# Performance work log

Measured on AMD Instinct MI355X. Metric: run time of the kernel, lower is better.

The kernel has to match this reference:

```python
import jax, jax.numpy as jnp
import numpy as np

V, E, HID, L = 32000, 2048, 8192, 4
H, KV, DK, DH = 16, 4, 128, 128
SEQ, WINDOW = 2048, 1024
EPS = 1e-5


def rms_norm(x):
    return x * jax.lax.rsqrt(jnp.mean(x * x, axis=-1, keepdims=True) + EPS)


def rope_buffers(seq_len, key_size):
    half = key_size // 2
    offset = jnp.arange(key_size) % half
    scales = jnp.power(10000.0, -2.0 / key_size * offset.astype(jnp.float32))
    angles = jnp.arange(seq_len, dtype=jnp.float32)[:, None] * scales[None, :]  # [S, DK]
    cos = jnp.cos(angles)
    sin = jnp.sin(angles)
    sin = sin.at[:, :half].multiply(-1.0)
    return cos, sin


def rotate(f, cos, sin):
    # f: [B, heads, S, DK]; cos/sin: [S, DK]
    half = DK // 2
    swapped = jnp.concatenate([f[..., half:], f[..., :half]], axis=-1)
    return cos * f + sin * swapped


def sliding_window_attention(q, k, v, window):
    # q: [B,H,S,DK], k: [B,KV,S,DK], v: [B,KV,S,DH]; GQA broadcast
    B, _, S, _ = q.shape
    G = H // KV
    qg = q.reshape(B, KV, G, S, DK)
    scores = jnp.einsum('bkgqd,bkjd->bkgqj', qg, k) / jnp.sqrt(jnp.asarray(DK, q.dtype))
    i = jnp.arange(S)[:, None]
    j = jnp.arange(S)[None, :]
    mask = (j <= i) & (i - j < window)
    scores = jnp.where(mask, scores, jnp.asarray(-1e9, scores.dtype))
    probs = jax.nn.softmax(scores, axis=-1)
    out = jnp.einsum('bkgqj,bkjd->bkgqd', probs, v)
    return out.reshape(B, H, S, DH)


def setup_inputs() -> dict:
    key = jax.random.key(0)
    ks = jax.random.split(key, 9)
    s = lambda k, shape, fan: jax.random.normal(k, shape, jnp.float32) / np.sqrt(fan)
    return {
        'tokens': jax.random.randint(ks[0], (1, SEQ), 0, V),
        'table': jax.random.normal(ks[1], (V, E), jnp.float32) * 0.02,
        'wq': s(ks[2], (L, E, H * DK), E),
        'wk': s(ks[3], (L, E, KV * DK), E),
        'wv': s(ks[4], (L, E, KV * DH), E),
        'wo': s(ks[5], (L, H * DH, E), H * DH),
        'w_up': s(ks[6], (L, E, 2 * HID), E),
        'w_down': s(ks[7], (L, HID, E), HID),
        'w_vocab': s(ks[8], (E, V), E),
    }


def reference(tokens, table, wq, wk, wv, wo, w_up, w_down, w_vocab):
    B, S = tokens.shape
    table = table.at[0].set(0.0)  # forward zeroes row 0 each call
    cos, sin = rope_buffers(S, DK)
    x = table[tokens]  # [B, S, E]
    for l in range(L):
        # --- self attention ---
        n = rms_norm(x)
        q = (n @ wq[l]).reshape(B, S, H, DK).transpose(0, 2, 1, 3)
        k = (n @ wk[l]).reshape(B, S, KV, DK).transpose(0, 2, 1, 3)
        v = (n @ wv[l]).reshape(B, S, KV, DH).transpose(0, 2, 1, 3)
        q = rotate(q, cos, sin)
        k = rotate(k, cos, sin)
        attn = sliding_window_attention(q, k, v, WINDOW)
        attn = attn.transpose(0, 2, 1, 3).reshape(B, S, H * DH)
        x = x + attn @ wo[l]
        # --- SwiGLU FFN ---
        n = rms_norm(x)
        gu = n @ w_up[l]
        gate, up = gu[..., :HID], gu[..., HID:]
        x = x + (up * jax.nn.silu(gate)) @ w_down[l]
    x = rms_norm(x)
    logits = x @ w_vocab  # [B, S, V]
    return logits
```

## Files before the change

### kernel.cpp

```cpp
#include <hip/hip_runtime.h>
#include <cstdint>

typedef unsigned short bf16u;
typedef __attribute__((ext_vector_type(8))) short short8;
typedef __attribute__((ext_vector_type(4))) short short4v;
typedef __attribute__((ext_vector_type(4))) float f32x4;

#define SEQ   2048
#define EMB   2048
#define NHEAD 16
#define NKV   4
#define DKH   128
#define HIDN  8192
#define NVOC  32000
#define NLAY  4
#define WIN   1024
#define QKV_N 3072

__device__ __forceinline__ bf16u f2bf(float f) {
  union { float f; uint32_t u; } v; v.f = f;
  uint32_t r = v.u + 0x7FFFu + ((v.u >> 16) & 1u);
  return (bf16u)(r >> 16);
}
__device__ __forceinline__ float bf2f(bf16u b) {
  union { uint32_t u; float f; } v; v.u = ((uint32_t)b) << 16;
  return v.f;
}

__device__ __forceinline__ void gl2lds16(const void* g, void* l) {
  __builtin_amdgcn_global_load_lds(
      (const __attribute__((address_space(1))) void*)g,
      (__attribute__((address_space(3))) void*)l, 16, 0, 0);
}

__global__ __launch_bounds__(256) void embed_kernel(const int* __restrict__ tokens,
                                                    const float* __restrict__ table,
                                                    float* __restrict__ x) {
  int s = blockIdx.x;
  int tok = tokens[s];
  int i0 = threadIdx.x * 8;
  float4 a = {0,0,0,0}, b = {0,0,0,0};
  if (tok != 0) {
    const float* src = table + (size_t)tok * EMB;
    a = *(const float4*)(src + i0);
    b = *(const float4*)(src + i0 + 4);
  }
  *(float4*)(x + (size_t)s * EMB + i0) = a;
  *(float4*)(x + (size_t)s * EMB + i0 + 4) = b;
}

__global__ __launch_bounds__(256) void rmsnorm_kernel(const float* __restrict__ x,
                                                      bf16u* __restrict__ out) {
  int s = blockIdx.x;
  const float* row = x + (size_t)s * EMB;
  int i0 = threadIdx.x * 8;
  float4 a = *(const float4*)(row + i0);
  float4 b = *(const float4*)(row + i0 + 4);
  float ss = a.x*a.x + a.y*a.y + a.z*a.z + a.w*a.w
           + b.x*b.x + b.y*b.y + b.z*b.z + b.w*b.w;
  #pragma unroll
  for (int off = 1; off < 64; off <<= 1) ss += __shfl_xor(ss, off);
  __shared__ float red[4];
  if ((threadIdx.x & 63) == 0) red[threadIdx.x >> 6] = ss;
  __syncthreads();
  float scale = rsqrtf((red[0] + red[1] + red[2] + red[3]) * (1.0f / EMB) + 1e-5f);
  float v[8] = {a.x, a.y, a.z, a.w, b.x, b.y, b.z, b.w};
  short8 o;
  #pragma unroll
  for (int j = 0; j < 8; ++j) o[j] = (short)f2bf(v[j] * scale);
  *(short8*)(out + (size_t)s * EMB + i0) = o;
}

__global__ __launch_bounds__(256) void reduce4norm_kernel(float* __restrict__ x,
                                                          const float* __restrict__ p,
                                                          bf16u* __restrict__ nout) {
  int s = blockIdx.x;
  const size_t MN = (size_t)SEQ * EMB;
  size_t base = (size_t)s * EMB + threadIdx.x * 8;
  float v[8];
  #pragma unroll
  for (int h = 0; h < 2; ++h) {
    size_t i = base + h * 4;
    float4 a  = *(const float4*)(x + i);
    float4 b0 = *(const float4*)(p + i);
    float4 b1 = *(const float4*)(p + i + MN);
    float4 b2 = *(const float4*)(p + i + 2 * MN);
    float4 b3 = *(const float4*)(p + i + 3 * MN);
    v[h*4+0] = a.x + b0.x + b1.x + b2.x + b3.x;
    v[h*4+1] = a.y + b0.y + b1.y + b2.y + b3.y;
    v[h*4+2] = a.z + b0.z + b1.z + b2.z + b3.z;
    v[h*4+3] = a.w + b0.w + b1.w + b2.w + b3.w;
    *(float4*)(x + i) = make_float4(v[h*4+0], v[h*4+1], v[h*4+2], v[h*4+3]);
  }
  float ss = 0.0f;
  #pragma unroll
  for (int j = 0; j < 8; ++j) ss += v[j] * v[j];
  #pragma unroll
  for (int off = 1; off < 64; off <<= 1) ss += __shfl_xor(ss, off);
  __shared__ float red[4];
  if ((threadIdx.x & 63) == 0) red[threadIdx.x >> 6] = ss;
  __syncthreads();
  float scale = rsqrtf((red[0] + red[1] + red[2] + red[3]) * (1.0f / EMB) + 1e-5f);
  short8 o;
  #pragma unroll
  for (int j = 0; j < 8; ++j) o[j] = (short)f2bf(v[j] * scale);
  *(short8*)(nout + base) = o;
}

__global__ __launch_bounds__(256) void transp_kernel(const float* __restrict__ in,
                                                     bf16u* __restrict__ out,
                                                     int R, int C, int pairhalf,
                                                     size_t ostride) {
  __shared__ float tile[64][65];
  in  += (size_t)blockIdx.z * R * C;
  out += (size_t)blockIdx.z * ostride;
  int c0 = blockIdx.x * 64, r0 = blockIdx.y * 64;
  int tx = threadIdx.x & 15, ty = threadIdx.x >> 4;
  #pragma unroll
  for (int i = 0; i < 4; ++i) {
    int r = ty + i * 16;
    float4 v = *(const float4*)(in + (size_t)(r0 + r) * C + c0 + tx * 4);
    tile[tx * 4 + 0][r] = v.x;
    tile[tx * 4 + 1][r] = v.y;
    tile[tx * 4 + 2][r] = v.z;
    tile[tx * 4 + 3][r] = v.w;
  }
  __syncthreads();
  int rx = threadIdx.x & 15, cy = threadIdx.x >> 4;
  #pragma unroll
  for (int i = 0; i < 4; ++i) {
    int c = c0 + cy + i * 16;
    int n = pairhalf ? (c < pairhalf ? 2 * c : 2 * (c - pairhalf) + 1) : c;
    short4v o;
    #pragma unroll
    for (int j = 0; j < 4; ++j) o[j] = (short)f2bf(tile[cy + i * 16][rx * 4 + j]);
    *(short4v*)(out + (size_t)n * R + r0 + rx * 4) = o;
  }
}

__global__ __launch_bounds__(256) void rope_kernel(const bf16u* __restrict__ qkv,
                                                   bf16u* __restrict__ q_bf,
                                                   bf16u* __restrict__ k_bf) {
  int idx = blockIdx.x * 256 + threadIdx.x;
  int d = idx & 63;
  int s = (idx >> 6) & (SEQ - 1);
  int h = idx >> 17;
  int col0 = (h < NHEAD) ? h * DKH : 2048 + (h - NHEAD) * DKH;
  const bf16u* row = qkv + (size_t)s * QKV_N + col0;
  float ang = (float)s * __powf(10000.0f, -(float)d * (1.0f / 64.0f));
  float si, c;
  sincosf(ang, &si, &c);
  float f0 = bf2f(row[d]), f1 = bf2f(row[d + 64]);
  bf16u* orow = (h < NHEAD) ? q_bf + ((size_t)h * SEQ + s) * DKH
                            : k_bf + ((size_t)(h - NHEAD) * SEQ + s) * DKH;
  orow[d]      = f2bf(c * f0 - si * f1);
  orow[d + 64] = f2bf(c * f1 + si * f0);
}

template <int MODE>
__global__ __launch_bounds__(256) void gemm_kernel(const bf16u* __restrict__ A,
                                                   const bf16u* __restrict__ Bt,
                                                   void* __restrict__ C,
                                                   int M, int N, int K) {
  __shared__ __align__(16) char lds[2][2][8192];

  int nx = gridDim.x, ny = gridDim.y;
  int nwg = nx * ny;
  int orig = blockIdx.y * nx + blockIdx.x;
  int q = nwg >> 3, r = nwg & 7;
  int xcd = orig & 7, loc = orig >> 3;
  int id = (xcd < r ? xcd * (q + 1) : r * (q + 1) + (xcd - r) * q) + loc;
  int bx = id / ny, by = id - bx * ny;
  int n0 = bx * 128, m0 = by * 128;

  int t = threadIdx.x;
  int w = t >> 6, l = t & 63;
  int wm = (w >> 1) * 64, wn = (w & 1) * 64;
  int l15 = l & 15, l4 = l >> 4;

  int srow = w * 16 + (l >> 2);
  int scol = (l & 3) * 8;

  f32x4 acc[4][4] = {};

  auto stage = [&](int buf, int k0) {
    #pragma unroll
    for (int i = 0; i < 2; ++i) {
      gl2lds16(A  + (size_t)(m0 + i * 64 + srow) * K + k0 + scol,
               &lds[buf][0][i * 4096 + w * 1024]);
      gl2lds16(Bt + (size_t)(n0 + i * 64 + srow) * K + k0 + scol,
               &lds[buf][1][i * 4096 + w * 1024]);
    }
  };

  auto compute = [&](int buf) {
    short8 af[4], bfr[4];
    #pragma unroll
    for (int i = 0; i < 4; ++i) {
      af[i]  = *(const short8*)(&lds[buf][0][((wm + i * 16 + l15) * 32 + l4 * 8) * 2]);
      bfr[i] = *(const short8*)(&lds[buf][1][((wn + i * 16 + l15) * 32 + l4 * 8) * 2]);
    }
    #pragma unroll
    for (int i = 0; i < 4; ++i)
      #pragma unroll
      for (int j = 0; j < 4; ++j)
        acc[i][j] = __builtin_amdgcn_mfma_f32_16x16x32_bf16(af[i], bfr[j], acc[i][j], 0, 0, 0);
  };

  int nt = K >> 5;
  int cur = 0;
  stage(0, 0);
  __syncthreads();
  for (int tt = 0; tt < nt; ++tt) {
    if (tt + 1 < nt) stage(cur ^ 1, (tt + 1) * 32);
    compute(cur);
    __syncthreads();
    cur ^= 1;
  }

  #pragma unroll
  for (int i = 0; i < 4; ++i)
    #pragma unroll
    for (int j = 0; j < 4; ++j) {
      int col = n0 + wn + j * 16 + l15;
      #pragma unroll
      for (int rr = 0; rr < 4; ++rr) {
        int row = m0 + wm + i * 16 + l4 * 4 + rr;
        float v = acc[i][j][rr];
        if (MODE == 0) {
          ((bf16u*)C)[(size_t)row * N + col] = f2bf(v);
        } else if (MODE == 1) {
          float* p = (float*)C + (size_t)row * N + col;
          *p += v;
        } else {
          ((float*)C)[(size_t)row * N + col] = v;
        }
      }
    }
}

__device__ __forceinline__ void stage_half(const bf16u* __restrict__ p, int ld,
                                           int row0, int k0, char* slotBase, int t) {
  int r  = t >> 3, c8 = t & 7;
  int cs = (c8 ^ (r & 7)) << 3;
  gl2lds16(p + (size_t)(row0 + r) * ld + k0 + cs, slotBase + t * 16);
  gl2lds16(p + (size_t)(row0 + 64 + r) * ld + k0 + cs, slotBase + 8192 + t * 16);
}

template<int KK>
__device__ __forceinline__ short8 read_frag(const char* slot, int row, int l4) {
  int kc = KK * 4 + l4;
  return *(const short8*)(slot + row * 128 + ((kc ^ (row & 7)) << 4));
}

template<int NH>
__device__ __forceinline__ void mfma_quad(f32x4 (&acc)[8][4], const short8 (&a)[8],
                                          short8 b0, short8 b1) {
  __builtin_amdgcn_s_setprio(1);
  #pragma unroll
  for (int mi = 0; mi < 8; ++mi) {
    acc[mi][NH * 2]     = __builtin_amdgcn_mfma_f32_16x16x32_bf16(a[mi], b0, acc[mi][NH * 2], 0, 0, 0);
    acc[mi][NH * 2 + 1] = __builtin_amdgcn_mfma_f32_16x16x32_bf16(a[mi], b1, acc[mi][NH * 2 + 1], 0, 0, 0);
  }
  __builtin_amdgcn_s_setprio(0);
}

template <int MODE>
__global__ __launch_bounds__(512) void gemm256_kernel(const bf16u* __restrict__ A,
                                                      const bf16u* __restrict__ Bt,
                                                      void* __restrict__ C,
                                                      int M, int N, int K, int ldk) {
  __shared__ __align__(16) char lds[131072];

  int koff = blockIdx.z * K;
  A  += koff;
  Bt += koff;
  float* Cz = (float*)C + (size_t)blockIdx.z * M * N;

  int nx = gridDim.x, ny = gridDim.y;
  int nwg = nx * ny;
  int orig = blockIdx.y * nx + blockIdx.x;
  int q8 = nwg >> 3, r8 = nwg & 7;
  int xcd = orig & 7, loc = orig >> 3;
  int id = (xcd < r8 ? xcd * (q8 + 1) : r8 * (q8 + 1) + (xcd - r8) * q8) + loc;
  int bx = id / ny, by = id - bx * ny;
  int n0 = bx * 256, m0 = by * 256;

  int t = threadIdx.x;
  int wid = t >> 6, lane = t & 63;
  int wr = wid >> 2, wc = wid & 3, bh = wc >> 1;
  int l15 = lane & 15, l4 = lane >> 4;

  char* AS0 = lds;              char* AS1 = lds + 16384;
  char* AS2 = lds + 32768;      char* AS3 = lds + 49152;
  char* BS0 = lds + 65536;      char* BS1 = lds + 81920;
  char* BS2 = lds + 98304;      char* BS3 = lds + 114688;

  const char* ASe = lds + wr * 16384;
  const char* ASo = ASe + 32768;
  const char* BSe = lds + 65536 + bh * 16384;
  const char* BSo = BSe + 32768;

  int brow = (wc & 1) * 64;

  f32x4 acc[8][4] = {};
  short8 a[8];
  short8 b0, b1;

  int NT = K >> 6;
  int NI = NT >> 1;

  stage_half(A,  ldk, m0,       0,  AS0, t);
  stage_half(A,  ldk, m0 + 128, 0,  AS1, t);
  stage_half(Bt, ldk, n0,       0,  BS0, t);
  stage_half(Bt, ldk, n0 + 128, 0,  BS1, t);
  stage_half(A,  ldk, m0,       64, AS2, t);
  asm volatile("s_waitcnt vmcnt(2)" ::: "memory");
  __builtin_amdgcn_s_barrier();
  __builtin_amdgcn_sched_barrier(0);

  for (int I = 0; I < NI; ++I) {
    int t0k = I * 128;
    int t1k = t0k + 64;
    bool notlast = (I + 1 < NI);

    #pragma unroll
    for (int mi = 0; mi < 8; ++mi) a[mi] = read_frag<0>(ASe, mi * 16 + l15, l4);
    b0 = read_frag<0>(BSe, brow + l15, l4);
    b1 = read_frag<0>(BSe, brow + 16 + l15, l4);
    stage_half(A, ldk, m0 + 128, t1k, AS3, t);
    __builtin_amdgcn_s_barrier();
    mfma_quad<0>(acc, a, b0, b1);
    __builtin_amdgcn_s_barrier();

    b0 = read_frag<0>(BSe, brow + 32 + l15, l4);
    b1 = read_frag<0>(BSe, brow + 48 + l15, l4);
    stage_half(Bt, ldk, n0, t1k, BS2, t);
    __builtin_amdgcn_s_barrier();
    mfma_quad<1>(acc, a, b0, b1);
    __builtin_amdgcn_s_barrier();

    #pragma unroll
    for (int mi = 0; mi < 8; ++mi) a[mi] = read_frag<1>(ASe, mi * 16 + l15, l4);
    b0 = read_frag<1>(BSe, brow + l15, l4);
    b1 = read_frag<1>(BSe, brow + 16 + l15, l4);
    stage_half(Bt, ldk, n0 + 128, t1k, BS3, t);
    __builtin_amdgcn_s_barrier();
    mfma_quad<0>(acc, a, b0, b1);
    __builtin_amdgcn_s_barrier();

    b0 = read_frag<1>(BSe, brow + 32 + l15, l4);
    b1 = read_frag<1>(BSe, brow + 48 + l15, l4);
    if (notlast) stage_half(A, ldk, m0, t0k + 128, AS0, t);
    if (notlast) { asm volatile("s_waitcnt vmcnt(2)" ::: "memory"); }
    else         { asm volatile("s_waitcnt vmcnt(0)" ::: "memory"); }
    __builtin_amdgcn_s_barrier();
    __builtin_amdgcn_sched_barrier(0);
    mfma_quad<1>(acc, a, b0, b1);
    __builtin_amdgcn_s_barrier();

    #pragma unroll
    for (int mi = 0; mi < 8; ++mi) a[mi] = read_frag<0>(ASo, mi * 16 + l15, l4);
    b0 = read_frag<0>(BSo, brow + l15, l4);
    b1 = read_frag<0>(BSo, brow + 16 + l15, l4);
    if (notlast) stage_half(A, ldk, m0 + 128, t0k + 128, AS1, t);
    __builtin_amdgcn_s_barrier();
    mfma_quad<0>(acc, a, b0, b1);
    __builtin_amdgcn_s_barrier();

    b0 = read_frag<0>(BSo, brow + 32 + l15, l4);
    b1 = read_frag<0>(BSo, brow + 48 + l15, l4);
    if (notlast) stage_half(Bt, ldk, n0, t0k + 128, BS0, t);
    __builtin_amdgcn_s_barrier();
    mfma_quad<1>(acc, a, b0, b1);
    __builtin_amdgcn_s_barrier();

    #pragma unroll
    for (int mi = 0; mi < 8; ++mi) a[mi] = read_frag<1>(ASo, mi * 16 + l15, l4);
    b0 = read_frag<1>(BSo, brow + l15, l4);
    b1 = read_frag<1>(BSo, brow + 16 + l15, l4);
    if (notlast) stage_half(Bt, ldk, n0 + 128, t0k + 128, BS1, t);
    __builtin_amdgcn_s_barrier();
    mfma_quad<0>(acc, a, b0, b1);
    __builtin_amdgcn_s_barrier();

    b0 = read_frag<1>(BSo, brow + 32 + l15, l4);
    b1 = read_frag<1>(BSo, brow + 48 + l15, l4);
    if (notlast) {
      stage_half(A, ldk, m0, t0k + 192, AS2, t);
      asm volatile("s_waitcnt vmcnt(2)" ::: "memory");
    }
    __builtin_amdgcn_s_barrier();
    __builtin_amdgcn_sched_barrier(0);
    mfma_quad<1>(acc, a, b0, b1);
    __builtin_amdgcn_s_barrier();
  }

  #pragma unroll
  for (int mi = 0; mi < 8; ++mi)
    #pragma unroll
    for (int ni = 0; ni < 4; ++ni) {
      int col = n0 + wc * 64 + ni * 16 + l15;
      #pragma unroll
      for (int rr = 0; rr < 4; ++rr) {
        int row = m0 + wr * 128 + mi * 16 + l4 * 4 + rr;
        float v = acc[mi][ni][rr];
        if (MODE == 3) {
          float pv = __shfl_xor(v, 1);
          if ((l15 & 1) == 0) {
            float hval = pv * (v / (1.0f + __expf(-v)));
            ((bf16u*)C)[(size_t)row * HIDN + (col >> 1)] = f2bf(hval);
          }
        } else if (MODE == 2) {
          Cz[(size_t)row * N + col] = v;
        } else if (MODE == 1) {
          float* p = (float*)C + (size_t)row * N + col;
          *p += v;
        } else {
          ((bf16u*)C)[(size_t)row * N + col] = f2bf(v);
        }
      }
    }
}

__global__ __launch_bounds__(512) void attn_kernel(const bf16u* __restrict__ q_bf,
                                                   const bf16u* __restrict__ k_bf,
                                                   const bf16u* __restrict__ qkv_bf,
                                                   bf16u* __restrict__ attn_out) {
  int h = blockIdx.y;
  int q0 = blockIdx.x * 128;
  int kvh = h >> 2;
  const bf16u* Kp = k_bf + (size_t)kvh * SEQ * DKH;
  const bf16u* Vp = qkv_bf + 2560 + kvh * DKH;

  __shared__ __align__(16) char  Klds[64 * 128 * 2];
  __shared__ __align__(16) bf16u Vlds[128][72];
  __shared__ __align__(16) bf16u Plds[8][16][72];

  int t = threadIdx.x, wave = t >> 6, lane = t & 63;
  int l15 = lane & 15, l4 = lane >> 4;
  int qrow0 = q0 + wave * 16;

  short8 qf[4];
  #pragma unroll
  for (int ks = 0; ks < 4; ++ks)
    qf[ks] = *(const short8*)(q_bf + ((size_t)h * SEQ + qrow0 + l15) * DKH + ks * 32 + l4 * 8);

  f32x4 o[8] = {};
  float m[4], lsum[4];
  #pragma unroll
  for (int r = 0; r < 4; ++r) { m[r] = -INFINITY; lsum[r] = 0.0f; }

  int vkey = t & 63, vd0 = (t >> 6) * 16;

  int jstart = q0 >= WIN ? ((q0 - (WIN - 1)) & ~63) : 0;

  for (int j0 = jstart; j0 < q0 + 128; j0 += 64) {
    __syncthreads();
    #pragma unroll
    for (int i = 0; i < 2; ++i) {
      int c = t + i * 512;
      int key = c >> 4, cc = c & 15;
      int off = key * 256 + cc * 16; off ^= (key & 7) << 4;
      *(short8*)(Klds + off) = *(const short8*)(Kp + (size_t)(j0 + key) * DKH + cc * 8);
    }
    {
      const bf16u* src = Vp + (size_t)(j0 + vkey) * QKV_N + vd0;
      short8 v0 = *(const short8*)(src);
      short8 v1 = *(const short8*)(src + 8);
      #pragma unroll
      for (int i = 0; i < 8; ++i) Vlds[vd0 + i][vkey] = (bf16u)(unsigned short)v0[i];
      #pragma unroll
      for (int i = 0; i < 8; ++i) Vlds[vd0 + 8 + i][vkey] = (bf16u)(unsigned short)v1[i];
    }
    __syncthreads();

    f32x4 sacc[4] = {};
    #pragma unroll
    for (int nt = 0; nt < 4; ++nt) {
      int key = nt * 16 + l15;
      #pragma unroll
      for (int ks = 0; ks < 4; ++ks) {
        int off = key * 256 + ks * 64 + l4 * 16; off ^= (key & 7) << 4;
        short8 kf = *(short8*)(Klds + off);
        sacc[nt] = __builtin_amdgcn_mfma_f32_16x16x32_bf16(qf[ks], kf, sacc[nt], 0, 0, 0);
      }
    }

    float sv[4][4];
    #pragma unroll
    for (int nt = 0; nt < 4; ++nt) {
      int jk = j0 + nt * 16 + l15;
      #pragma unroll
      for (int r = 0; r < 4; ++r) {
        int iq = qrow0 + l4 * 4 + r;
        float s = sacc[nt][r] * 0.08838834764831845f;
        bool valid = (jk <= iq) && (iq - jk < WIN);
        sv[nt][r] = valid ? s : -1e9f;
      }
    }

    float mxr[4];
    #pragma unroll
    for (int r = 0; r < 4; ++r) {
      float mx = fmaxf(fmaxf(sv[0][r], sv[1][r]), fmaxf(sv[2][r], sv[3][r]));
      #pragma unroll
      for (int off = 1; off < 16; off <<= 1) mx = fmaxf(mx, __shfl_xor(mx, off));
      mxr[r] = mx;
    }

    bool grow = (mxr[0] > m[0] + 8.0f) || (mxr[1] > m[1] + 8.0f) ||
                (mxr[2] > m[2] + 8.0f) || (mxr[3] > m[3] + 8.0f);
    if (__any(grow)) {
      #pragma unroll
      for (int r = 0; r < 4; ++r) {
        float mn = fmaxf(m[r], mxr[r]);
        float alpha = __expf(m[r] - mn);
        m[r] = mn;
        lsum[r] *= alpha;
        #pragma unroll
        for (int d = 0; d < 8; ++d) o[d][r] *= alpha;
      }
    }

    float p[4][4];
    #pragma unroll
    for (int r = 0; r < 4; ++r) {
      float ps = 0.0f;
      #pragma unroll
      for (int nt = 0; nt < 4; ++nt) { p[nt][r] = __expf(sv[nt][r] - m[r]); ps += p[nt][r]; }
      #pragma unroll
      for (int off = 1; off < 16; off <<= 1) ps += __shfl_xor(ps, off);
      lsum[r] += ps;
    }

    #pragma unroll
    for (int nt = 0; nt < 4; ++nt)
      #pragma unroll
      for (int r = 0; r < 4; ++r)
        Plds[wave][l4 * 4 + r][nt * 16 + l15] = f2bf(p[nt][r]);

    #pragma unroll
    for (int kk = 0; kk < 2; ++kk) {
      short8 pf = *(short8*)(&Plds[wave][l15][kk * 32 + l4 * 8]);
      #pragma unroll
      for (int d = 0; d < 8; ++d) {
        short8 vf = *(short8*)(&Vlds[d * 16 + l15][kk * 32 + l4 * 8]);
        o[d] = __builtin_amdgcn_mfma_f32_16x16x32_bf16(pf, vf, o[d], 0, 0, 0);
      }
    }
  }

  #pragma unroll
  for (int d = 0; d < 8; ++d)
    #pragma unroll
    for (int r = 0; r < 4; ++r) {
      int row = qrow0 + l4 * 4 + r;
      attn_out[(size_t)row * (NHEAD * DKH) + h * DKH + d * 16 + l15] = f2bf(o[d][r] / lsum[r]);
    }
}

extern "C" void kernel_launch(void* const* d_in, const int* in_sizes, int n_in,
                              void* d_out, int out_size, void* d_ws, size_t ws_size,
                              hipStream_t stream) {
  const int*   tokens  = (const int*)d_in[0];
  const float* table   = (const float*)d_in[1];
  const float* wq      = (const float*)d_in[2];
  const float* wk      = (const float*)d_in[3];
  const float* wv      = (const float*)d_in[4];
  const float* wo      = (const float*)d_in[5];
  const float* w_up    = (const float*)d_in[6];
  const float* w_down  = (const float*)d_in[7];
  const float* w_vocab = (const float*)d_in[8];
  float* out = (float*)d_out;

  char* base = (char*)d_ws;
  size_t o = 0;
  auto alloc = [&](size_t bytes) { size_t r = o; o += (bytes + 255) & ~(size_t)255; return r; };
  size_t o_x     = alloc((size_t)SEQ * EMB * 4);
  size_t o_nbf   = alloc((size_t)SEQ * EMB * 2);
  size_t o_qkvw  = alloc((size_t)NLAY * QKV_N * EMB * 2);
  size_t o_wot   = alloc((size_t)NLAY * EMB * EMB * 2);
  size_t o_wupt  = alloc((size_t)NLAY * 2 * HIDN * EMB * 2);
  size_t o_wdnt  = alloc((size_t)NLAY * EMB * HIDN * 2);
  size_t o_qkvbf = alloc((size_t)SEQ * QKV_N * 2);
  size_t o_qbf   = alloc((size_t)NHEAD * SEQ * DKH * 2);
  size_t o_kbf   = alloc((size_t)NKV * SEQ * DKH * 2);
  size_t o_attn  = alloc((size_t)SEQ * EMB * 2);
  size_t o_big   = alloc((size_t)SEQ * 2 * HIDN * 4);
  size_t o_hbf   = alloc((size_t)SEQ * HIDN * 2);

  float* x      = (float*)(base + o_x);
  bf16u* n_bf   = (bf16u*)(base + o_nbf);
  bf16u* qkvw_t = (bf16u*)(base + o_qkvw);
  bf16u* wo_t   = (bf16u*)(base + o_wot);
  bf16u* wup_t  = (bf16u*)(base + o_wupt);
  bf16u* wdn_t  = (bf16u*)(base + o_wdnt);
  bf16u* qkv_bf = (bf16u*)(base + o_qkvbf);
  bf16u* q_bf   = (bf16u*)(base + o_qbf);
  bf16u* k_bf   = (bf16u*)(base + o_kbf);
  bf16u* attn_b = (bf16u*)(base + o_attn);
  float* part   = (float*)(base + o_big);
  bf16u* h_bf   = (bf16u*)(base + o_hbf);
  bf16u* wvoc_t = (bf16u*)(base + o_big);

  const size_t QKVW = (size_t)QKV_N * EMB;

  transp_kernel<<<dim3(EMB / 64, EMB / 64, NLAY), 256, 0, stream>>>(
      wq, qkvw_t, EMB, EMB, 0, QKVW);
  transp_kernel<<<dim3(512 / 64, EMB / 64, NLAY), 256, 0, stream>>>(
      wk, qkvw_t + (size_t)2048 * EMB, EMB, 512, 0, QKVW);
  transp_kernel<<<dim3(512 / 64, EMB / 64, NLAY), 256, 0, stream>>>(
      wv, qkvw_t + (size_t)2560 * EMB, EMB, 512, 0, QKVW);
  transp_kernel<<<dim3(EMB / 64, EMB / 64, NLAY), 256, 0, stream>>>(
      wo, wo_t, EMB, EMB, 0, (size_t)EMB * EMB);
  transp_kernel<<<dim3(2 * HIDN / 64, EMB / 64, NLAY), 256, 0, stream>>>(
      w_up, wup_t, EMB, 2 * HIDN, HIDN, (size_t)2 * HIDN * EMB);
  transp_kernel<<<dim3(EMB / 64, HIDN / 64, NLAY), 256, 0, stream>>>(
      w_down, wdn_t, HIDN, EMB, 0, (size_t)EMB * HIDN);

  embed_kernel<<<SEQ, 256, 0, stream>>>(tokens, table, x);
  rmsnorm_kernel<<<SEQ, 256, 0, stream>>>(x, n_bf);

  for (int l = 0; l < NLAY; ++l) {
    gemm_kernel<0><<<dim3(QKV_N / 128, SEQ / 128), 256, 0, stream>>>(
        n_bf, qkvw_t + (size_t)l * QKVW, qkv_bf, SEQ, QKV_N, EMB);

    rope_kernel<<<(NHEAD + NKV) * SEQ * 64 / 256, 256, 0, stream>>>(qkv_bf, q_bf, k_bf);

    attn_kernel<<<dim3(SEQ / 128, NHEAD), 512, 0, stream>>>(q_bf, k_bf, qkv_bf, attn_b);

    gemm_kernel<1><<<dim3(EMB / 128, SEQ / 128), 256, 0, stream>>>(
        attn_b, wo_t + (size_t)l * EMB * EMB, x, SEQ, EMB, EMB);

    rmsnorm_kernel<<<SEQ, 256, 0, stream>>>(x, n_bf);
    gemm256_kernel<3><<<dim3(2 * HIDN / 256, SEQ / 256), 512, 0, stream>>>(
        n_bf, wup_t + (size_t)l * 2 * HIDN * EMB, h_bf, SEQ, 2 * HIDN, EMB, EMB);
    gemm256_kernel<2><<<dim3(EMB / 256, SEQ / 256, 4), 512, 0, stream>>>(
        h_bf, wdn_t + (size_t)l * EMB * HIDN, part, SEQ, EMB, 2048, HIDN);
    reduce4norm_kernel<<<SEQ, 256, 0, stream>>>(x, part, n_bf);
  }

  transp_kernel<<<dim3(NVOC / 64, EMB / 64, 1), 256, 0, stream>>>(
      w_vocab, wvoc_t, EMB, NVOC, 0, 0);
  gemm256_kernel<2><<<dim3(NVOC / 256, SEQ / 256), 512, 0, stream>>>(
      n_bf, wvoc_t, out, SEQ, NVOC, EMB, EMB);
}
```

Before: 2.349 ms.

## Fuse RoPE into attention, precompute rope table, split KV range across two blocks

Removes the separate rope kernel. A sin/cos table is now computed once per forward, and the rotation is applied to Q and K as they are loaded inside the attention kernel. Attention now splits each query tile's key range into two halves along a new grid z dimension, which doubles the number of blocks. Each block writes unnormalized fp32 partial outputs plus max and sum statistics, and a new combine kernel merges them into bf16. The cost is extra fp32 partial traffic, one extra launch per layer, and K being re-rotated by every head that shares it.

Result: slower. 2.399 ms (+2.1%).

```diff
diff --git a/kernel.cpp b/kernel.cpp
--- a/kernel.cpp
+++ b/kernel.cpp
@@ -47,6 +47,17 @@
   }
   *(float4*)(x + (size_t)s * EMB + i0) = a;
   *(float4*)(x + (size_t)s * EMB + i0 + 4) = b;
+}
+
+__global__ __launch_bounds__(256) void ropetab_kernel(float* __restrict__ tab) {
+  int idx = blockIdx.x * 256 + threadIdx.x;
+  int d = idx & 63;
+  int s = idx >> 6;
+  float ang = (float)s * __powf(10000.0f, -(float)d * (1.0f / 64.0f));
+  float si, c;
+  sincosf(ang, &si, &c);
+  tab[(size_t)s * 128 + d] = c;
+  tab[(size_t)s * 128 + 64 + d] = si;
 }
 
 __global__ __launch_bounds__(256) void rmsnorm_kernel(const float* __restrict__ x,
@@ -136,25 +147,6 @@
     for (int j = 0; j < 4; ++j) o[j] = (short)f2bf(tile[cy + i * 16][rx * 4 + j]);
     *(short4v*)(out + (size_t)n * R + r0 + rx * 4) = o;
   }
-}
-
-__global__ __launch_bounds__(256) void rope_kernel(const bf16u* __restrict__ qkv,
-                                                   bf16u* __restrict__ q_bf,
-                                                   bf16u* __restrict__ k_bf) {
-  int idx = blockIdx.x * 256 + threadIdx.x;
-  int d = idx & 63;
-  int s = (idx >> 6) & (SEQ - 1);
-  int h = idx >> 17;
-  int col0 = (h < NHEAD) ? h * DKH : 2048 + (h - NHEAD) * DKH;
-  const bf16u* row = qkv + (size_t)s * QKV_N + col0;
-  float ang = (float)s * __powf(10000.0f, -(float)d * (1.0f / 64.0f));
-  float si, c;
-  sincosf(ang, &si, &c);
-  float f0 = bf2f(row[d]), f1 = bf2f(row[d + 64]);
-  bf16u* orow = (h < NHEAD) ? q_bf + ((size_t)h * SEQ + s) * DKH
-                            : k_bf + ((size_t)(h - NHEAD) * SEQ + s) * DKH;
-  orow[d]      = f2bf(c * f0 - si * f1);
-  orow[d + 64] = f2bf(c * f1 + si * f0);
 }
 
 template <int MODE>
@@ -423,15 +415,16 @@
     }
 }
 
-__global__ __launch_bounds__(512) void attn_kernel(const bf16u* __restrict__ q_bf,
-                                                   const bf16u* __restrict__ k_bf,
-                                                   const bf16u* __restrict__ qkv_bf,
-                                                   bf16u* __restrict__ attn_out) {
+__global__ __launch_bounds__(512) void attn_kernel(const bf16u* __restrict__ qkv_bf,
+                                                   const float* __restrict__ tab,
+                                                   float* __restrict__ opart,
+                                                   float* __restrict__ mlbuf) {
   int h = blockIdx.y;
   int q0 = blockIdx.x * 128;
+  int z = blockIdx.z;
   int kvh = h >> 2;
-  const bf16u* Kp = k_bf + (size_t)kvh * SEQ * DKH;
-  const bf16u* Vp = qkv_bf + 2560 + kvh * DKH;
+  const bf16u* Kg = qkv_bf + 2048 + kvh * DKH;
+  const bf16u* Vg = qkv_bf + 2560 + kvh * DKH;
 
   __shared__ __align__(16) char  Klds[64 * 128 * 2];
   __shared__ __align__(16) bf16u Vlds[128][72];
@@ -441,10 +434,32 @@
   int l15 = lane & 15, l4 = lane >> 4;
   int qrow0 = q0 + wave * 16;
 
+  int qrow = qrow0 + l15;
   short8 qf[4];
-  #pragma unroll
-  for (int ks = 0; ks < 4; ++ks)
-    qf[ks] = *(const short8*)(q_bf + ((size_t)h * SEQ + qrow0 + l15) * DKH + ks * 32 + l4 * 8);
+  {
+    short8 qr[4];
+    #pragma unroll
+    for (int ks = 0; ks < 4; ++ks)
+      qr[ks] = *(const short8*)(qkv_bf + (size_t)qrow * QKV_N + h * DKH + ks * 32 + l4 * 8);
+    #pragma unroll
+    for (int hf = 0; hf < 2; ++hf) {
+      int dbase = hf * 32 + l4 * 8;
+      const float* tc = tab + (size_t)qrow * 128 + dbase;
+      float4 c0 = *(const float4*)(tc);
+      float4 c1 = *(const float4*)(tc + 4);
+      float4 s0 = *(const float4*)(tc + 64);
+      float4 s1 = *(const float4*)(tc + 68);
+      float cc[8] = {c0.x,c0.y,c0.z,c0.w,c1.x,c1.y,c1.z,c1.w};
+      float ssn[8] = {s0.x,s0.y,s0.z,s0.w,s1.x,s1.y,s1.z,s1.w};
+      #pragma unroll
+      for (int j = 0; j < 8; ++j) {
+        float f0 = bf2f((bf16u)(unsigned short)qr[hf][j]);
+        float f1 = bf2f((bf16u)(unsigned short)qr[hf + 2][j]);
+        qf[hf][j]     = (short)f2bf(cc[j] * f0 - ssn[j] * f1);
+        qf[hf + 2][j] = (short)f2bf(cc[j] * f1 + ssn[j] * f0);
+      }
+    }
+  }
 
   f32x4 o[8] = {};
   float m[4], lsum[4];
@@ -452,20 +467,43 @@
   for (int r = 0; r < 4; ++r) { m[r] = -INFINITY; lsum[r] = 0.0f; }
 
   int vkey = t & 63, vd0 = (t >> 6) * 16;
+  int kkey = t & 63, kd0 = (t >> 6) * 8;
 
   int jstart = q0 >= WIN ? ((q0 - (WIN - 1)) & ~63) : 0;
-
-  for (int j0 = jstart; j0 < q0 + 128; j0 += 64) {
+  int T  = (q0 + 128 - jstart) >> 6;
+  int T0 = T >> 1;
+  int jb = jstart + (z ? T0 * 64 : 0);
+  int je = z ? (jstart + T * 64) : (jstart + T0 * 64);
+
+  for (int j0 = jb; j0 < je; j0 += 64) {
     __syncthreads();
-    #pragma unroll
-    for (int i = 0; i < 2; ++i) {
-      int c = t + i * 512;
-      int key = c >> 4, cc = c & 15;
-      int off = key * 256 + cc * 16; off ^= (key & 7) << 4;
-      *(short8*)(Klds + off) = *(const short8*)(Kp + (size_t)(j0 + key) * DKH + cc * 8);
-    }
     {
-      const bf16u* src = Vp + (size_t)(j0 + vkey) * QKV_N + vd0;
+      int srow = j0 + kkey;
+      const bf16u* src = Kg + (size_t)srow * QKV_N + kd0;
+      short8 r0 = *(const short8*)(src);
+      short8 r1 = *(const short8*)(src + 64);
+      const float* tc = tab + (size_t)srow * 128 + kd0;
+      float4 c0 = *(const float4*)(tc);
+      float4 c1 = *(const float4*)(tc + 4);
+      float4 s0 = *(const float4*)(tc + 64);
+      float4 s1 = *(const float4*)(tc + 68);
+      float cc[8] = {c0.x,c0.y,c0.z,c0.w,c1.x,c1.y,c1.z,c1.w};
+      float ssn[8] = {s0.x,s0.y,s0.z,s0.w,s1.x,s1.y,s1.z,s1.w};
+      short8 o0, o1;
+      #pragma unroll
+      for (int j = 0; j < 8; ++j) {
+        float f0 = bf2f((bf16u)(unsigned short)r0[j]);
+        float f1 = bf2f((bf16u)(unsigned short)r1[j]);
+        o0[j] = (short)f2bf(cc[j] * f0 - ssn[j] * f1);
+        o1[j] = (short)f2bf(cc[j] * f1 + ssn[j] * f0);
+      }
+      int cl = (kd0 >> 3) ^ (kkey & 7);
+      int ch = 8 + ((kd0 >> 3) ^ (kkey & 7));
+      *(short8*)(Klds + kkey * 256 + cl * 16) = o0;
+      *(short8*)(Klds + kkey * 256 + ch * 16) = o1;
+    }
+    {
+      const bf16u* src = Vg + (size_t)(j0 + vkey) * QKV_N + vd0;
       short8 v0 = *(const short8*)(src);
       short8 v1 = *(const short8*)(src + 8);
       #pragma unroll
@@ -551,13 +589,50 @@
     }
   }
 
+  float* op = opart + (((size_t)z * NHEAD + h) * SEQ) * DKH;
   #pragma unroll
   for (int d = 0; d < 8; ++d)
     #pragma unroll
     for (int r = 0; r < 4; ++r) {
       int row = qrow0 + l4 * 4 + r;
-      attn_out[(size_t)row * (NHEAD * DKH) + h * DKH + d * 16 + l15] = f2bf(o[d][r] / lsum[r]);
-    }
+      op[(size_t)row * DKH + d * 16 + l15] = o[d][r];
+    }
+  if (l15 == 0) {
+    float* ml = mlbuf + ((size_t)z * NHEAD + h) * SEQ * 2;
+    #pragma unroll
+    for (int r = 0; r < 4; ++r) {
+      int row = qrow0 + l4 * 4 + r;
+      ml[(size_t)row * 2]     = m[r];
+      ml[(size_t)row * 2 + 1] = lsum[r];
+    }
+  }
+}
+
+__global__ __launch_bounds__(256) void combine_kernel(const float* __restrict__ opart,
+                                                      const float* __restrict__ mlbuf,
+                                                      bf16u* __restrict__ attn_out) {
+  size_t idx = ((size_t)blockIdx.x * 256 + threadIdx.x) * 4;
+  int d4 = (int)(idx & 127);
+  int s  = (int)((idx >> 7) & (SEQ - 1));
+  int h  = (int)(idx >> 18);
+  const size_t OSZ = (size_t)NHEAD * SEQ * DKH;
+  const float* o1 = opart + ((size_t)h * SEQ + s) * DKH + d4;
+  const float* o2 = o1 + OSZ;
+  const float* ml1 = mlbuf + ((size_t)h * SEQ + s) * 2;
+  const float* ml2 = ml1 + (size_t)NHEAD * SEQ * 2;
+  float m1 = ml1[0], l1 = ml1[1];
+  float m2 = ml2[0], l2 = ml2[1];
+  float ms = fmaxf(m1, m2);
+  float a1 = __expf(m1 - ms), a2 = __expf(m2 - ms);
+  float inv = 1.0f / (a1 * l1 + a2 * l2);
+  float4 v1 = *(const float4*)o1;
+  float4 v2 = *(const float4*)o2;
+  short4v o;
+  o[0] = (short)f2bf((a1 * v1.x + a2 * v2.x) * inv);
+  o[1] = (short)f2bf((a1 * v1.y + a2 * v2.y) * inv);
+  o[2] = (short)f2bf((a1 * v1.z + a2 * v2.z) * inv);
+  o[3] = (short)f2bf((a1 * v1.w + a2 * v2.w) * inv);
+  *(short4v*)(attn_out + (size_t)s * EMB + h * DKH + d4) = o;
 }
 
 extern "C" void kernel_launch(void* const* d_in, const int* in_sizes, int n_in,
@@ -584,8 +659,7 @@
   size_t o_wupt  = alloc((size_t)NLAY * 2 * HIDN * EMB * 2);
   size_t o_wdnt  = alloc((size_t)NLAY * EMB * HIDN * 2);
   size_t o_qkvbf = alloc((size_t)SEQ * QKV_N * 2);
-  size_t o_qbf   = alloc((size_t)NHEAD * SEQ * DKH * 2);
-  size_t o_kbf   = alloc((size_t)NKV * SEQ * DKH * 2);
+  size_t o_tab   = alloc((size_t)SEQ * 128 * 4);
   size_t o_attn  = alloc((size_t)SEQ * EMB * 2);
   size_t o_big   = alloc((size_t)SEQ * 2 * HIDN * 4);
   size_t o_hbf   = alloc((size_t)SEQ * HIDN * 2);
@@ -597,10 +671,11 @@
   bf16u* wup_t  = (bf16u*)(base + o_wupt);
   bf16u* wdn_t  = (bf16u*)(base + o_wdnt);
   bf16u* qkv_bf = (bf16u*)(base + o_qkvbf);
-  bf16u* q_bf   = (bf16u*)(base + o_qbf);
-  bf16u* k_bf   = (bf16u*)(base + o_kbf);
+  float* ropetb = (float*)(base + o_tab);
   bf16u* attn_b = (bf16u*)(base + o_attn);
   float* part   = (float*)(base + o_big);
+  float* opart  = (float*)(base + o_big);
+  float* mlbuf  = (float*)(base + o_big + (size_t)2 * NHEAD * SEQ * DKH * 4);
   bf16u* h_bf   = (bf16u*)(base + o_hbf);
   bf16u* wvoc_t = (bf16u*)(base + o_big);
 
@@ -619,6 +694,7 @@
   transp_kernel<<<dim3(EMB / 64, HIDN / 64, NLAY), 256, 0, stream>>>(
       w_down, wdn_t, HIDN, EMB, 0, (size_t)EMB * HIDN);
 
+  ropetab_kernel<<<SEQ * 64 / 256, 256, 0, stream>>>(ropetb);
   embed_kernel<<<SEQ, 256, 0, stream>>>(tokens, table, x);
   rmsnorm_kernel<<<SEQ, 256, 0, stream>>>(x, n_bf);
 
@@ -626,9 +702,10 @@
     gemm_kernel<0><<<dim3(QKV_N / 128, SEQ / 128), 256, 0, stream>>>(
         n_bf, qkvw_t + (size_t)l * QKVW, qkv_bf, SEQ, QKV_N, EMB);
 
-    rope_kernel<<<(NHEAD + NKV) * SEQ * 64 / 256, 256, 0, stream>>>(qkv_bf, q_bf, k_bf);
-
-    attn_kernel<<<dim3(SEQ / 128, NHEAD), 512, 0, stream>>>(q_bf, k_bf, qkv_bf, attn_b);
+    attn_kernel<<<dim3(SEQ / 128, NHEAD, 2), 512, 0, stream>>>(
+        qkv_bf, ropetb, opart, mlbuf);
+    combine_kernel<<<NHEAD * SEQ * DKH / 1024, 256, 0, stream>>>(
+        opart, mlbuf, attn_b);
 
     gemm_kernel<1><<<dim3(EMB / 128, SEQ / 128), 256, 0, stream>>>(
         attn_b, wo_t + (size_t)l * EMB * EMB, x, SEQ, EMB, EMB);
```

## Split attention KV range across two blocks with combine pass; fuse embed and norm

Applied to the files above, without the earlier changes.

The attention grid gains a second z dimension that splits each query tile's key range in half. Each half writes unnormalized fp32 partial outputs plus running max and sum, and a new combine kernel merges them into bf16. This raises block count from 256 to 512 to improve CU occupancy on a 256-CU part, at the cost of extra fp32 traffic and one more launch per layer. The embedding lookup and the first RMSNorm are also fused into one kernel to save a launch and a re-read of x.

Result: faster. 2.290 ms (-2.5%).

```diff
diff --git a/kernel.cpp b/kernel.cpp
--- a/kernel.cpp
+++ b/kernel.cpp
@@ -33,20 +33,35 @@
       (__attribute__((address_space(3))) void*)l, 16, 0, 0);
 }
 
-__global__ __launch_bounds__(256) void embed_kernel(const int* __restrict__ tokens,
-                                                    const float* __restrict__ table,
-                                                    float* __restrict__ x) {
+__global__ __launch_bounds__(256) void embednorm_kernel(const int* __restrict__ tokens,
+                                                        const float* __restrict__ table,
+                                                        float* __restrict__ x,
+                                                        bf16u* __restrict__ nout) {
   int s = blockIdx.x;
   int tok = tokens[s];
   int i0 = threadIdx.x * 8;
-  float4 a = {0,0,0,0}, b = {0,0,0,0};
+  float v[8] = {0,0,0,0,0,0,0,0};
   if (tok != 0) {
     const float* src = table + (size_t)tok * EMB;
-    a = *(const float4*)(src + i0);
-    b = *(const float4*)(src + i0 + 4);
-  }
-  *(float4*)(x + (size_t)s * EMB + i0) = a;
-  *(float4*)(x + (size_t)s * EMB + i0 + 4) = b;
+    float4 a = *(const float4*)(src + i0);
+    float4 b = *(const float4*)(src + i0 + 4);
+    v[0]=a.x; v[1]=a.y; v[2]=a.z; v[3]=a.w; v[4]=b.x; v[5]=b.y; v[6]=b.z; v[7]=b.w;
+  }
+  *(float4*)(x + (size_t)s * EMB + i0)     = make_float4(v[0],v[1],v[2],v[3]);
+  *(float4*)(x + (size_t)s * EMB + i0 + 4) = make_float4(v[4],v[5],v[6],v[7]);
+  float ss = 0.0f;
+  #pragma unroll
+  for (int j = 0; j < 8; ++j) ss += v[j] * v[j];
+  #pragma unroll
+  for (int off = 1; off < 64; off <<= 1) ss += __shfl_xor(ss, off);
+  __shared__ float red[4];
+  if ((threadIdx.x & 63) == 0) red[threadIdx.x >> 6] = ss;
+  __syncthreads();
+  float scale = rsqrtf((red[0] + red[1] + red[2] + red[3]) * (1.0f / EMB) + 1e-5f);
+  short8 o;
+  #pragma unroll
+  for (int j = 0; j < 8; ++j) o[j] = (short)f2bf(v[j] * scale);
+  *(short8*)(nout + (size_t)s * EMB + i0) = o;
 }
 
 __global__ __launch_bounds__(256) void rmsnorm_kernel(const float* __restrict__ x,
@@ -426,9 +441,11 @@
 __global__ __launch_bounds__(512) void attn_kernel(const bf16u* __restrict__ q_bf,
                                                    const bf16u* __restrict__ k_bf,
                                                    const bf16u* __restrict__ qkv_bf,
-                                                   bf16u* __restrict__ attn_out) {
+                                                   float* __restrict__ opart,
+                                                   float* __restrict__ mlbuf) {
   int h = blockIdx.y;
   int q0 = blockIdx.x * 128;
+  int z = blockIdx.z;
   int kvh = h >> 2;
   const bf16u* Kp = k_bf + (size_t)kvh * SEQ * DKH;
   const bf16u* Vp = qkv_bf + 2560 + kvh * DKH;
@@ -454,8 +471,12 @@
   int vkey = t & 63, vd0 = (t >> 6) * 16;
 
   int jstart = q0 >= WIN ? ((q0 - (WIN - 1)) & ~63) : 0;
-
-  for (int j0 = jstart; j0 < q0 + 128; j0 += 64) {
+  int T  = (q0 + 128 - jstart) >> 6;
+  int T0 = T >> 1;
+  int jb = jstart + (z ? T0 * 64 : 0);
+  int je = z ? (jstart + T * 64) : (jstart + T0 * 64);
+
+  for (int j0 = jb; j0 < je; j0 += 64) {
     __syncthreads();
     #pragma unroll
     for (int i = 0; i < 2; ++i) {
@@ -551,13 +572,50 @@
     }
   }
 
+  float* op = opart + (((size_t)z * NHEAD + h) * SEQ) * DKH;
   #pragma unroll
   for (int d = 0; d < 8; ++d)
     #pragma unroll
     for (int r = 0; r < 4; ++r) {
       int row = qrow0 + l4 * 4 + r;
-      attn_out[(size_t)row * (NHEAD * DKH) + h * DKH + d * 16 + l15] = f2bf(o[d][r] / lsum[r]);
-    }
+      op[(size_t)row * DKH + d * 16 + l15] = o[d][r];
+    }
+  if (l15 == 0) {
+    float* ml = mlbuf + ((size_t)z * NHEAD + h) * SEQ * 2;
+    #pragma unroll
+    for (int r = 0; r < 4; ++r) {
+      int row = qrow0 + l4 * 4 + r;
+      ml[(size_t)row * 2]     = m[r];
+      ml[(size_t)row * 2 + 1] = lsum[r];
+    }
+  }
+}
+
+__global__ __launch_bounds__(256) void combine_kernel(const float* __restrict__ opart,
+                                                      const float* __restrict__ mlbuf,
+                                                      bf16u* __restrict__ attn_out) {
+  size_t idx = ((size_t)blockIdx.x * 256 + threadIdx.x) * 4;
+  int d4 = (int)(idx & 127);
+  int s  = (int)((idx >> 7) & (SEQ - 1));
+  int h  = (int)(idx >> 18);
+  const size_t OSZ = (size_t)NHEAD * SEQ * DKH;
+  const float* o1 = opart + ((size_t)h * SEQ + s) * DKH + d4;
+  const float* o2 = o1 + OSZ;
+  const float* ml1 = mlbuf + ((size_t)h * SEQ + s) * 2;
+  const float* ml2 = ml1 + (size_t)NHEAD * SEQ * 2;
+  float m1 = ml1[0], l1 = ml1[1];
+  float m2 = ml2[0], l2 = ml2[1];
+  float ms = fmaxf(m1, m2);
+  float a1 = __expf(m1 - ms), a2 = __expf(m2 - ms);
+  float inv = 1.0f / (a1 * l1 + a2 * l2);
+  float4 v1 = *(const float4*)o1;
+  float4 v2 = *(const float4*)o2;
+  short4v o;
+  o[0] = (short)f2bf((a1 * v1.x + a2 * v2.x) * inv);
+  o[1] = (short)f2bf((a1 * v1.y + a2 * v2.y) * inv);
+  o[2] = (short)f2bf((a1 * v1.z + a2 * v2.z) * inv);
+  o[3] = (short)f2bf((a1 * v1.w + a2 * v2.w) * inv);
+  *(short4v*)(attn_out + (size_t)s * EMB + h * DKH + d4) = o;
 }
 
 extern "C" void kernel_launch(void* const* d_in, const int* in_sizes, int n_in,
@@ -601,6 +659,8 @@
   bf16u* k_bf   = (bf16u*)(base + o_kbf);
   bf16u* attn_b = (bf16u*)(base + o_attn);
   float* part   = (float*)(base + o_big);
+  float* opart  = (float*)(base + o_big);
+  float* mlbuf  = (float*)(base + o_big + (size_t)2 * NHEAD * SEQ * DKH * 4);
   bf16u* h_bf   = (bf16u*)(base + o_hbf);
   bf16u* wvoc_t = (bf16u*)(base + o_big);
 
@@ -619,8 +679,7 @@
   transp_kernel<<<dim3(EMB / 64, HIDN / 64, NLAY), 256, 0, stream>>>(
       w_down, wdn_t, HIDN, EMB, 0, (size_t)EMB * HIDN);
 
-  embed_kernel<<<SEQ, 256, 0, stream>>>(tokens, table, x);
-  rmsnorm_kernel<<<SEQ, 256, 0, stream>>>(x, n_bf);
+  embednorm_kernel<<<SEQ, 256, 0, stream>>>(tokens, table, x, n_bf);
 
   for (int l = 0; l < NLAY; ++l) {
     gemm_kernel<0><<<dim3(QKV_N / 128, SEQ / 128), 256, 0, stream>>>(
@@ -628,7 +687,10 @@
 
     rope_kernel<<<(NHEAD + NKV) * SEQ * 64 / 256, 256, 0, stream>>>(qkv_bf, q_bf, k_bf);
 
-    attn_kernel<<<dim3(SEQ / 128, NHEAD), 512, 0, stream>>>(q_bf, k_bf, qkv_bf, attn_b);
+    attn_kernel<<<dim3(SEQ / 128, NHEAD, 2), 512, 0, stream>>>(
+        q_bf, k_bf, qkv_bf, opart, mlbuf);
+    combine_kernel<<<NHEAD * SEQ * DKH / 1024, 256, 0, stream>>>(
+        opart, mlbuf, attn_b);
 
     gemm_kernel<1><<<dim3(EMB / 128, SEQ / 128), 256, 0, stream>>>(
         attn_b, wo_t + (size_t)l * EMB * EMB, x, SEQ, EMB, EMB);
```
